# Kernel tuning notes

Measured on AMD Instinct MI355X. Metric: run time of the kernel, lower is better.

The kernel has to match this reference:

```python
import jax, jax.numpy as jnp
import numpy as np
from jax import lax

X_SIZE, Z_SIZE, H, GC, PD = 256, 64, 64, 16, 2
B, K, T = 256, 16, 50
LOG_SIG_MIN, LOG_SIG_MAX, LOG_P_MAX = -10.0, 10.0, 50.0
ZX = X_SIZE + Z_SIZE
LSTM_IN = ZX + PD


def setup_inputs() -> dict:
    key = jax.random.key(0)
    ks = jax.random.split(key, 24)
    s = lambda fan_in: 1.0 / np.sqrt(fan_in)
    u = lambda k, shape, sc: jax.random.uniform(k, shape, jnp.float32, -sc, sc)
    inp = {
        'x': jax.random.normal(ks[0], (B, X_SIZE), jnp.float32),
        'z_stacked': jax.random.normal(ks[1], (K, B, Z_SIZE), jnp.float32),
        'input_seqs': jax.random.normal(ks[2], (B, 8, 2, 2, 6), jnp.float32),
        'pred_seqs': jax.random.normal(ks[3], (B, T, 2, 2, 6), jnp.float32),
        # initial_h / initial_c linears: ZX -> H
        'Wh0': u(ks[4], (H, ZX), s(ZX)), 'bh0': u(ks[5], (H,), s(ZX)),
        'Wc0': u(ks[6], (H, ZX), s(ZX)), 'bc0': u(ks[7], (H,), s(ZX)),
        # LSTMCell: gates order i,f,g,o
        'Wih': u(ks[8], (4 * H, LSTM_IN), s(H)), 'Whh': u(ks[9], (4 * H, H), s(H)),
        'bih': u(ks[10], (4 * H,), s(H)), 'bhh': u(ks[11], (4 * H,), s(H)),
        # GMM parameter heads: H -> GC / GC*PD
        'Wpi': u(ks[12], (GC, H), s(H)), 'bpi': u(ks[13], (GC,), s(H)),
        'Wmu': u(ks[14], (GC * PD, H), s(H)), 'bmu': u(ks[15], (GC * PD,), s(H)),
        'Wls': u(ks[16], (GC * PD, H), s(H)), 'bls': u(ks[17], (GC * PD,), s(H)),
        'Wcorr': u(ks[18], (GC, H), s(H)), 'bcorr': u(ks[19], (GC,), s(H)),
        'n_z_samples': K,
    }
    return inp


def _gmm2d_log_prob(log_pis, mus, log_sigmas, corrs, value):
    # log_pis/corrs: [K,B,T,GC]; mus/log_sigmas: [K,B,T,GC*PD]; value: [B,T,PD]
    ls = jnp.clip(log_sigmas, LOG_SIG_MIN, LOG_SIG_MAX).reshape(K, B, T, GC, PD)
    mu = mus.reshape(K, B, T, GC, PD)
    dx = value[None, :, :, None, :] - mu                      # [K,B,T,GC,PD]
    zscore = dx * jnp.exp(-ls)                                # dx / sigma
    one_m_rho2 = 1.0 - corrs ** 2
    quad = (zscore[..., 0] ** 2 + zscore[..., 1] ** 2
            - 2.0 * corrs * zscore[..., 0] * zscore[..., 1])
    comp = (-jnp.log(2.0 * jnp.pi) - ls.sum(-1)
            - 0.5 * jnp.log(one_m_rho2) - 0.5 * quad / one_m_rho2)
    log_pi_n = jax.nn.log_softmax(log_pis, axis=-1)
    log_p_t = jax.nn.logsumexp(log_pi_n + comp, axis=-1)      # [K,B,T]
    return jnp.minimum(log_p_t, LOG_P_MAX)


def reference(x, z_stacked, input_seqs, pred_seqs,
              Wh0, bh0, Wc0, bc0, Wih, Whh, bih, bhh,
              Wpi, bpi, Wmu, bmu, Wls, bls, Wcorr, bcorr, n_z_samples):
    tgt_future = pred_seqs[:, :, 1, 1, 2:4]                   # [B,T,2]
    tgt_present = input_seqs[:, -1, 1, 1, 2:4]                # [B,2]
    z = z_stacked.reshape(-1, z_stacked.shape[-1])            # [K*B, z]
    zx = jnp.concatenate([z, jnp.tile(x, (n_z_samples, 1))], axis=1)  # [N, ZX]
    N = zx.shape[0]
    h0 = zx @ Wh0.T + bh0
    c0 = zx @ Wc0.T + bc0
    decode_inputs = jnp.concatenate([tgt_present[:, None, :], tgt_future[:, :T - 1, :]], axis=1)  # [B,T,2]
    inputs = jnp.concatenate([
        jnp.broadcast_to(zx[:, None, :], (N, T, ZX)),
        jnp.tile(decode_inputs, (n_z_samples, 1, 1))], axis=2)  # [N,T,ZX+2]

    def step(carry, xt):
        h, c = carry
        gates = xt @ Wih.T + bih + h @ Whh.T + bhh
        i, f, g, o = jnp.split(gates, 4, axis=-1)
        c = jax.nn.sigmoid(f) * c + jax.nn.sigmoid(i) * jnp.tanh(g)
        h = jax.nn.sigmoid(o) * jnp.tanh(c)
        return (h, c), h

    _, hs = lax.scan(step, (h0, c0), jnp.swapaxes(inputs, 0, 1))  # [T,N,H]
    hs = jnp.swapaxes(hs, 0, 1)                                   # [N,T,H]

    log_pis = (hs @ Wpi.T + bpi).reshape(K, B, T, GC)
    mus = (hs @ Wmu.T + bmu).reshape(K, B, T, GC * PD)
    log_sigmas = (hs @ Wls.T + bls).reshape(K, B, T, GC * PD)
    corrs = jnp.tanh(hs @ Wcorr.T + bcorr).reshape(K, B, T, GC)

    log_p_yt_xz = _gmm2d_log_prob(log_pis, mus, log_sigmas, corrs, tgt_future)
    return log_p_yt_xz.sum(axis=2)                                # [K,B]
```

## Files before the change

kernel.cpp:

```cpp
#include <hip/hip_runtime.h>


#define T_ 50
#define SPB 16
#define ZXS 324
#define HFS 72
#define PLS 100

typedef __attribute__((ext_vector_type(8))) short short8;
typedef __attribute__((ext_vector_type(4))) float f32x4;

#define MFMA(a, b, c) __builtin_amdgcn_mfma_f32_16x16x32_bf16(a, b, c, 0, 0, 0)

__device__ __forceinline__ float sigf(float x)  { return 1.0f / (1.0f + __expf(-x)); }
__device__ __forceinline__ float tanh_(float x) { return 1.0f - 2.0f / (__expf(2.0f * x) + 1.0f); }

__device__ __forceinline__ void splitf(float f, unsigned short& hi, unsigned short& lo) {
    unsigned b = __float_as_uint(f);
    hi = (unsigned short)(b >> 16);
    float fh = __uint_as_float(b & 0xffff0000u);
    lo = (unsigned short)(__float_as_uint(f - fh) >> 16);
}

__device__ __forceinline__ void pack8(const float* p, short8& hi, short8& lo) {
    #pragma unroll
    for (int e = 0; e < 8; ++e) {
        unsigned short h, l;
        splitf(p[e], h, l);
        hi[e] = (short)h; lo[e] = (short)l;
    }
}

__launch_bounds__(512, 1)
__global__ void decoder_kernel(
    const float* __restrict__ x,       const float* __restrict__ z,
    const float* __restrict__ inp_seqs,const float* __restrict__ pred_seqs,
    const float* __restrict__ Wh0,     const float* __restrict__ bh0,
    const float* __restrict__ Wc0,     const float* __restrict__ bc0,
    const float* __restrict__ Wih,     const float* __restrict__ Whh,
    const float* __restrict__ bih,     const float* __restrict__ bhh,
    const float* __restrict__ Wpi,     const float* __restrict__ bpi,
    const float* __restrict__ Wmu,     const float* __restrict__ bmu,
    const float* __restrict__ Wls,     const float* __restrict__ bls,
    const float* __restrict__ Wcorr,   const float* __restrict__ bcorr,
    float* __restrict__ out)
{
    __shared__ __align__(16) float smem[9248];
    float* ZXL = smem;
    float* PL0 = smem;
    float* PL1 = smem + 1600;
    unsigned short* HF0h = (unsigned short*)(smem + 5184);
    unsigned short* HF0l = HF0h + 1152;
    unsigned short* HF1h = HF0h + 2304;
    unsigned short* HF1l = HF0h + 3456;
    float* FUT = smem + 7616;
    float* PRS = smem + 9216;

    const int j = threadIdx.x;
    const int w = j >> 6;
    const int l = j & 63;
    const int g = l >> 4;
    const int c = l & 15;
    const int U = 16*(w & 3) + c;
    const int blk = blockIdx.x;

    for (int e = j; e < SPB*320; e += 512) {
        int s = e / 320, k = e - s*320;
        int n = blk*SPB + s, kk = n >> 8, b = n & 255;
        ZXL[s*ZXS + k] = (k < 64) ? z[(kk*256 + b)*64 + k] : x[b*256 + (k - 64)];
    }
    for (int e = j; e < T_*SPB; e += 512) {
        int t = e >> 4, s = e & 15;
        int b = (blk*SPB + s) & 255;
        float2 v = *reinterpret_cast<const float2*>(pred_seqs + b*1200 + t*24 + 20);
        FUT[t*32 + s*2] = v.x; FUT[t*32 + s*2 + 1] = v.y;
    }
    if (j < SPB) {
        int b = (blk*SPB + j) & 255;
        float2 v = *reinterpret_cast<const float2*>(inp_seqs + b*192 + 188);
        PRS[j*2] = v.x; PRS[j*2 + 1] = v.y;
    }
    __syncthreads();

    float cst[4];
    f32x4 gci, gcf, gcg, gco;
    float wdi0=0,wdi1=0,wdf0=0,wdf1=0,wdg0=0,wdg1=0,wdo0=0,wdo1=0;
    short8 WIh0,WIl0,WIh1,WIl1, WFh0,WFl0,WFh1,WFl1,
           WGh0,WGl0,WGh1,WGl1, WOh0,WOl0,WOh1,WOl1;
    short8 qAh0,qAl0,qAh1,qAl1, qBh0,qBl0,qBh1,qBl1;
    float biasA = 0.0f, biasB = 0.0f;
    int ptA = 0, nproj = 0;

    auto projrow = [&](int r3, const float*& p, float& b) {
        if      (r3 < 16) { p = Wpi   + r3*64;      b = bpi[r3]; }
        else if (r3 < 48) { p = Wmu   + (r3-16)*64; b = bmu[r3-16]; }
        else if (r3 < 80) { p = Wls   + (r3-48)*64; b = bls[r3-48]; }
        else              { p = Wcorr + (r3-80)*64; b = bcorr[r3-80]; }
    };

    if (w < 4) {
        const int R0 = U, R1 = 64 + U, R2 = 128 + U, R3 = 192 + U;
        {
            float bi_ = bih[R0] + bhh[R0], bf_ = bih[R1] + bhh[R1];
            float bg_ = bih[R2] + bhh[R2], bo_ = bih[R3] + bhh[R3];
            gci = (f32x4){bi_,bi_,bi_,bi_}; gcf = (f32x4){bf_,bf_,bf_,bf_};
            gcg = (f32x4){bg_,bg_,bg_,bg_}; gco = (f32x4){bo_,bo_,bo_,bo_};
        }
        float bc_ = bc0[U];
        f32x4 c0a = (f32x4){bc_, bc_, bc_, bc_};
        for (int ks = 0; ks < 10; ++ks) {
            int k0 = ks*32 + g*8;
            short8 ah, al, b0h,b0l, b1h,b1l, b2h,b2l, b3h,b3l, bch,bcl;
            pack8(&ZXL[c*ZXS + k0], ah, al);
            pack8(Wih + R0*322 + k0, b0h, b0l);
            pack8(Wih + R1*322 + k0, b1h, b1l);
            pack8(Wih + R2*322 + k0, b2h, b2l);
            pack8(Wih + R3*322 + k0, b3h, b3l);
            pack8(Wc0 + U*320 + k0, bch, bcl);
            gci = MFMA(ah,b0h,gci); gci = MFMA(ah,b0l,gci); gci = MFMA(al,b0h,gci);
            gcf = MFMA(ah,b1h,gcf); gcf = MFMA(ah,b1l,gcf); gcf = MFMA(al,b1h,gcf);
            gcg = MFMA(ah,b2h,gcg); gcg = MFMA(ah,b2l,gcg); gcg = MFMA(al,b2h,gcg);
            gco = MFMA(ah,b3h,gco); gco = MFMA(ah,b3l,gco); gco = MFMA(al,b3h,gco);
            c0a = MFMA(ah,bch,c0a); c0a = MFMA(ah,bcl,c0a); c0a = MFMA(al,bch,c0a);
        }
        #pragma unroll
        for (int r = 0; r < 4; ++r) cst[r] = c0a[r];
        wdi0 = Wih[R0*322+320]; wdi1 = Wih[R0*322+321];
        wdf0 = Wih[R1*322+320]; wdf1 = Wih[R1*322+321];
        wdg0 = Wih[R2*322+320]; wdg1 = Wih[R2*322+321];
        wdo0 = Wih[R3*322+320]; wdo1 = Wih[R3*322+321];
        pack8(Whh + R0*64 +      g*8, WIh0, WIl0); pack8(Whh + R0*64 + 32 + g*8, WIh1, WIl1);
        pack8(Whh + R1*64 +      g*8, WFh0, WFl0); pack8(Whh + R1*64 + 32 + g*8, WFh1, WFl1);
        pack8(Whh + R2*64 +      g*8, WGh0, WGl0); pack8(Whh + R2*64 + 32 + g*8, WGh1, WGl1);
        pack8(Whh + R3*64 +      g*8, WOh0, WOl0); pack8(Whh + R3*64 + 32 + g*8, WOh1, WOl1);
    } else {
        float bh_ = bh0[U];
        f32x4 h0a = (f32x4){bh_, bh_, bh_, bh_};
        for (int ks = 0; ks < 10; ++ks) {
            int k0 = ks*32 + g*8;
            short8 ah, al, bhh_, bhl_;
            pack8(&ZXL[c*ZXS + k0], ah, al);
            pack8(Wh0 + U*320 + k0, bhh_, bhl_);
            h0a = MFMA(ah,bhh_,h0a); h0a = MFMA(ah,bhl_,h0a); h0a = MFMA(al,bhh_,h0a);
        }
        #pragma unroll
        for (int r = 0; r < 4; ++r) {
            unsigned short hh, ll; splitf(h0a[r], hh, ll);
            HF0h[(4*g + r)*HFS + U] = hh;
            HF0l[(4*g + r)*HFS + U] = ll;
        }
        const int v = w - 4;
        nproj = (v < 2) ? 2 : 1;
        ptA = (v < 2) ? 2*v : (4 + (v - 2));
        {
            const float* p; projrow(ptA*16 + c, p, biasA);
            pack8(p +      g*8, qAh0, qAl0);
            pack8(p + 32 + g*8, qAh1, qAl1);
        }
        if (nproj == 2) {
            const float* p; projrow((ptA+1)*16 + c, p, biasB);
            pack8(p +      g*8, qBh0, qBl0);
            pack8(p + 32 + g*8, qBh1, qBl1);
        }
    }

    const int jj = j & 255;
    const int s3 = jj >> 4, g3 = jj & 15;
    float sum = 0.0f;

    auto do_proj = [&](const unsigned short* Hh, const unsigned short* Hl, float* PLw) {
        short8 ah0 = *reinterpret_cast<const short8*>(Hh + c*HFS +      g*8);
        short8 al0 = *reinterpret_cast<const short8*>(Hl + c*HFS +      g*8);
        short8 ah1 = *reinterpret_cast<const short8*>(Hh + c*HFS + 32 + g*8);
        short8 al1 = *reinterpret_cast<const short8*>(Hl + c*HFS + 32 + g*8);
        f32x4 pA = (f32x4){biasA, biasA, biasA, biasA};
        pA = MFMA(ah0,qAh0,pA); pA = MFMA(ah0,qAl0,pA); pA = MFMA(al0,qAh0,pA);
        pA = MFMA(ah1,qAh1,pA); pA = MFMA(ah1,qAl1,pA); pA = MFMA(al1,qAh1,pA);
        #pragma unroll
        for (int r = 0; r < 4; ++r) PLw[(4*g + r)*PLS + ptA*16 + c] = pA[r];
        if (nproj == 2) {
            f32x4 pB = (f32x4){biasB, biasB, biasB, biasB};
            pB = MFMA(ah0,qBh0,pB); pB = MFMA(ah0,qBl0,pB); pB = MFMA(al0,qBh0,pB);
            pB = MFMA(ah1,qBh1,pB); pB = MFMA(ah1,qBl1,pB); pB = MFMA(al1,qBh1,pB);
            #pragma unroll
            for (int r = 0; r < 4; ++r) PLw[(4*g + r)*PLS + (ptA+1)*16 + c] = pB[r];
        }
    };
    auto do_gmm = [&](const float* pl, const float* fut2) {
        const float* pls = pl + s3*PLS;
        float a_pi = pls[g3];
        float a_m0 = pls[16 + 2*g3], a_m1 = pls[17 + 2*g3];
        float l0   = pls[48 + 2*g3], l1   = pls[49 + 2*g3];
        float a_co = pls[80 + g3];
        float v0 = fut2[s3*2], v1 = fut2[s3*2 + 1];
        l0 = fminf(fmaxf(l0, -10.0f), 10.0f);
        l1 = fminf(fmaxf(l1, -10.0f), 10.0f);
        float z0 = (v0 - a_m0) * __expf(-l0);
        float z1 = (v1 - a_m1) * __expf(-l1);
        float ct = tanh_(a_co);
        float omr = 1.0f - ct*ct;
        float quad = z0*z0 + z1*z1 - 2.0f*ct*z0*z1;
        float comp = -1.8378770664093453f - (l0 + l1) - 0.5f*__logf(omr) - 0.5f*quad/omr;
        float a = a_pi + comp;
        float m1v = a, m2v = a_pi;
        #pragma unroll
        for (int off = 1; off < 16; off <<= 1) {
            m1v = fmaxf(m1v, __shfl_xor(m1v, off));
            m2v = fmaxf(m2v, __shfl_xor(m2v, off));
        }
        float e1 = __expf(a - m1v), e2 = __expf(a_pi - m2v);
        #pragma unroll
        for (int off = 1; off < 16; off <<= 1) {
            e1 += __shfl_xor(e1, off);
            e2 += __shfl_xor(e2, off);
        }
        float logp = (m1v + __logf(e1)) - (m2v + __logf(e2));
        sum += fminf(logp, 50.0f);
    };

    __syncthreads();

    for (int t = 0; t < T_; ++t) {
        const unsigned short* Hh = (t & 1) ? HF1h : HF0h;
        const unsigned short* Hl = (t & 1) ? HF1l : HF0l;
        if (w < 4) {
            unsigned short* Nh = (t & 1) ? HF0h : HF1h;
            unsigned short* Nl = (t & 1) ? HF0l : HF1l;
            short8 ah0 = *reinterpret_cast<const short8*>(Hh + c*HFS +      g*8);
            short8 al0 = *reinterpret_cast<const short8*>(Hl + c*HFS +      g*8);
            short8 ah1 = *reinterpret_cast<const short8*>(Hh + c*HFS + 32 + g*8);
            short8 al1 = *reinterpret_cast<const short8*>(Hl + c*HFS + 32 + g*8);
            const float* dptr = (t == 0) ? PRS : (FUT + (t-1)*32);
            f32x4 ai, af, ag, ao;
            #pragma unroll
            for (int r = 0; r < 4; ++r) {
                float2 dv = *reinterpret_cast<const float2*>(dptr + (4*g + r)*2);
                ai[r] = gci[r] + dv.x*wdi0 + dv.y*wdi1;
                af[r] = gcf[r] + dv.x*wdf0 + dv.y*wdf1;
                ag[r] = gcg[r] + dv.x*wdg0 + dv.y*wdg1;
                ao[r] = gco[r] + dv.x*wdo0 + dv.y*wdo1;
            }
            ai = MFMA(ah0,WIh0,ai); ai = MFMA(ah0,WIl0,ai); ai = MFMA(al0,WIh0,ai);
            ai = MFMA(ah1,WIh1,ai); ai = MFMA(ah1,WIl1,ai); ai = MFMA(al1,WIh1,ai);
            af = MFMA(ah0,WFh0,af); af = MFMA(ah0,WFl0,af); af = MFMA(al0,WFh0,af);
            af = MFMA(ah1,WFh1,af); af = MFMA(ah1,WFl1,af); af = MFMA(al1,WFh1,af);
            ag = MFMA(ah0,WGh0,ag); ag = MFMA(ah0,WGl0,ag); ag = MFMA(al0,WGh0,ag);
            ag = MFMA(ah1,WGh1,ag); ag = MFMA(ah1,WGl1,ag); ag = MFMA(al1,WGh1,ag);
            ao = MFMA(ah0,WOh0,ao); ao = MFMA(ah0,WOl0,ao); ao = MFMA(al0,WOh0,ao);
            ao = MFMA(ah1,WOh1,ao); ao = MFMA(ah1,WOl1,ao); ao = MFMA(al1,WOh1,ao);
            #pragma unroll
            for (int r = 0; r < 4; ++r) {
                float cc = sigf(af[r])*cst[r] + sigf(ai[r])*tanh_(ag[r]);
                cst[r] = cc;
                float hv = sigf(ao[r])*tanh_(cc);
                unsigned short hh, ll; splitf(hv, hh, ll);
                Nh[(4*g + r)*HFS + U] = hh;
                Nl[(4*g + r)*HFS + U] = ll;
            }
        } else {
            if (t >= 1) do_proj(Hh, Hl, (t & 1) ? PL1 : PL0);
            if (t >= 2) do_gmm((t & 1) ? PL0 : PL1, FUT + (t-2)*32);
        }
        __syncthreads();
    }

    if (w >= 4) {
        do_proj(HF0h, HF0l, PL0);
        do_gmm(PL1, FUT + 48*32);
    }
    __syncthreads();
    if (w >= 4) {
        do_gmm(PL0, FUT + 49*32);
        if (g3 == 0) out[blk*SPB + s3] = sum;
    }
}

extern "C" void kernel_launch(void* const* d_in, const int* in_sizes, int n_in,
                              void* d_out, int out_size, void* d_ws, size_t ws_size,
                              hipStream_t stream) {
    const float* x     = (const float*)d_in[0];
    const float* z     = (const float*)d_in[1];
    const float* iseq  = (const float*)d_in[2];
    const float* pseq  = (const float*)d_in[3];
    const float* Wh0   = (const float*)d_in[4];
    const float* bh0   = (const float*)d_in[5];
    const float* Wc0   = (const float*)d_in[6];
    const float* bc0   = (const float*)d_in[7];
    const float* Wih   = (const float*)d_in[8];
    const float* Whh   = (const float*)d_in[9];
    const float* bih   = (const float*)d_in[10];
    const float* bhh   = (const float*)d_in[11];
    const float* Wpi   = (const float*)d_in[12];
    const float* bpi   = (const float*)d_in[13];
    const float* Wmu   = (const float*)d_in[14];
    const float* bmu   = (const float*)d_in[15];
    const float* Wls   = (const float*)d_in[16];
    const float* bls   = (const float*)d_in[17];
    const float* Wcorr = (const float*)d_in[18];
    const float* bcorr = (const float*)d_in[19];
    float* out = (float*)d_out;

    decoder_kernel<<<256, 512, 0, stream>>>(x, z, iseq, pseq, Wh0, bh0, Wc0, bc0,
                                            Wih, Whh, bih, bhh, Wpi, bpi, Wmu, bmu,
                                            Wls, bls, Wcorr, bcorr, out);
}
```

Before: 95.87 us.

## Split decoder block into 12 waves: dedicated LSTM, projection, and GMM waves

Grows the block from 8 to 12 waves. The initial zx projections (input gates, h0, c0) are spread evenly across all 12 waves, with intermediate results staged through shared memory. In the time loop, 4 waves run the LSTM cell, 4 run the GMM parameter projections, and 4 run the GMM log-prob, where the old code had one set of waves doing both projection and GMM. This shortens the serial prologue and lets projection and GMM work overlap per step, at the cost of extra barriers, more shared-memory reuse, and changed launch bounds that may limit registers per thread.

New measurement: 98.50 us. +2.7%, slower.

```diff
diff --git a/kernel.cpp b/kernel.cpp
--- a/kernel.cpp
+++ b/kernel.cpp
@@ -2,15 +2,9 @@
 
 
 #define T_ 50
-#define SPB 16
-#define ZXS 324
-#define HFS 72
-#define PLS 100
-
 typedef __attribute__((ext_vector_type(8))) short short8;
 typedef __attribute__((ext_vector_type(4))) float f32x4;
-
-#define MFMA(a, b, c) __builtin_amdgcn_mfma_f32_16x16x32_bf16(a, b, c, 0, 0, 0)
+#define MFMA(a,b,c) __builtin_amdgcn_mfma_f32_16x16x32_bf16(a,b,c,0,0,0)
 
 __device__ __forceinline__ float sigf(float x)  { return 1.0f / (1.0f + __expf(-x)); }
 __device__ __forceinline__ float tanh_(float x) { return 1.0f - 2.0f / (__expf(2.0f * x) + 1.0f); }
@@ -31,7 +25,7 @@
     }
 }
 
-__launch_bounds__(512, 1)
+__launch_bounds__(768, 3)
 __global__ void decoder_kernel(
     const float* __restrict__ x,       const float* __restrict__ z,
     const float* __restrict__ inp_seqs,const float* __restrict__ pred_seqs,
@@ -45,149 +39,168 @@
     const float* __restrict__ Wcorr,   const float* __restrict__ bcorr,
     float* __restrict__ out)
 {
-    __shared__ __align__(16) float smem[9248];
+    __shared__ __align__(16) float smem[7488];
     float* ZXL = smem;
+    float* gcX = smem;
+    float* c0X = smem + 4096;
     float* PL0 = smem;
     float* PL1 = smem + 1600;
+    float* FUT = smem + 3200;
+    float* PRS = smem + 4800;
     unsigned short* HF0h = (unsigned short*)(smem + 5184);
     unsigned short* HF0l = HF0h + 1152;
     unsigned short* HF1h = HF0h + 2304;
     unsigned short* HF1l = HF0h + 3456;
-    float* FUT = smem + 7616;
-    float* PRS = smem + 9216;
 
     const int j = threadIdx.x;
     const int w = j >> 6;
     const int l = j & 63;
     const int g = l >> 4;
     const int c = l & 15;
-    const int U = 16*(w & 3) + c;
     const int blk = blockIdx.x;
 
-    for (int e = j; e < SPB*320; e += 512) {
+    for (int e = j; e < 16*320; e += 768) {
         int s = e / 320, k = e - s*320;
-        int n = blk*SPB + s, kk = n >> 8, b = n & 255;
-        ZXL[s*ZXS + k] = (k < 64) ? z[(kk*256 + b)*64 + k] : x[b*256 + (k - 64)];
-    }
-    for (int e = j; e < T_*SPB; e += 512) {
-        int t = e >> 4, s = e & 15;
-        int b = (blk*SPB + s) & 255;
-        float2 v = *reinterpret_cast<const float2*>(pred_seqs + b*1200 + t*24 + 20);
-        FUT[t*32 + s*2] = v.x; FUT[t*32 + s*2 + 1] = v.y;
-    }
-    if (j < SPB) {
-        int b = (blk*SPB + j) & 255;
-        float2 v = *reinterpret_cast<const float2*>(inp_seqs + b*192 + 188);
-        PRS[j*2] = v.x; PRS[j*2 + 1] = v.y;
-    }
-    __syncthreads();
-
+        int n = blk*16 + s, b = n & 255;
+        ZXL[s*324 + k] = (k < 64) ? z[n*64 + k] : x[b*256 + (k - 64)];
+    }
+    __syncthreads();
+
+    const int tA = w;
+    f32x4 accA, accB;
+    const float* srcA;
+    const float* srcB;
+    int tB = -1;
+    {
+        int qA_ = tA >> 2, ubA_ = tA & 3;
+        int gaA = qA_*64 + 16*ubA_ + c;
+        float bA = bih[gaA] + bhh[gaA];
+        accA = (f32x4){bA, bA, bA, bA};
+        srcA = Wih + gaA*322;
+        float bB;
+        if (w < 4) {
+            tB = 12 + w;
+            int qB_ = tB >> 2, ubB_ = tB & 3;
+            int gaB = qB_*64 + 16*ubB_ + c;
+            bB = bih[gaB] + bhh[gaB];
+            srcB = Wih + gaB*322;
+        } else if (w < 8) {
+            int u = 16*(w-4) + c;
+            bB = bh0[u];
+            srcB = Wh0 + u*320;
+        } else {
+            int u = 16*(w-8) + c;
+            bB = bc0[u];
+            srcB = Wc0 + u*320;
+        }
+        accB = (f32x4){bB, bB, bB, bB};
+    }
+    for (int ks = 0; ks < 10; ++ks) {
+        short8 ah, al;
+        pack8(&ZXL[c*324 + ks*32 + g*8], ah, al);
+        short8 b1h, b1l; pack8(srcA + ks*32 + g*8, b1h, b1l);
+        accA = MFMA(ah, b1h, accA); accA = MFMA(ah, b1l, accA); accA = MFMA(al, b1h, accA);
+        short8 b2h, b2l; pack8(srcB + ks*32 + g*8, b2h, b2l);
+        accB = MFMA(ah, b2h, accB); accB = MFMA(ah, b2l, accB); accB = MFMA(al, b2h, accB);
+    }
+    __syncthreads();
+
+    #pragma unroll
+    for (int r = 0; r < 4; ++r) gcX[tA*256 + (4*g + r)*16 + c] = accA[r];
+    if (w < 4) {
+        #pragma unroll
+        for (int r = 0; r < 4; ++r) gcX[tB*256 + (4*g + r)*16 + c] = accB[r];
+    } else if (w < 8) {
+        #pragma unroll
+        for (int r = 0; r < 4; ++r) {
+            unsigned short hh, ll; splitf(accB[r], hh, ll);
+            HF0h[(4*g + r)*72 + 16*(w-4) + c] = hh;
+            HF0l[(4*g + r)*72 + 16*(w-4) + c] = ll;
+        }
+    } else {
+        #pragma unroll
+        for (int r = 0; r < 4; ++r) c0X[(4*g + r)*64 + 16*(w-8) + c] = accB[r];
+    }
+    __syncthreads();
+
+    f32x4 gc[4];
     float cst[4];
-    f32x4 gci, gcf, gcg, gco;
-    float wdi0=0,wdi1=0,wdf0=0,wdf1=0,wdg0=0,wdg1=0,wdo0=0,wdo1=0;
-    short8 WIh0,WIl0,WIh1,WIl1, WFh0,WFl0,WFh1,WFl1,
-           WGh0,WGl0,WGh1,WGl1, WOh0,WOl0,WOh1,WOl1;
-    short8 qAh0,qAl0,qAh1,qAl1, qBh0,qBl0,qBh1,qBl1;
-    float biasA = 0.0f, biasB = 0.0f;
+    short8 WH[4][2], WL[4][2];
+    float wd0[4], wd1[4];
+    short8 qAh0, qAl0, qAh1, qAl1, qBh0, qBl0, qBh1, qBl1;
+    float pbA = 0.0f, pbB = 0.0f;
     int ptA = 0, nproj = 0;
-
-    auto projrow = [&](int r3, const float*& p, float& b) {
-        if      (r3 < 16) { p = Wpi   + r3*64;      b = bpi[r3]; }
-        else if (r3 < 48) { p = Wmu   + (r3-16)*64; b = bmu[r3-16]; }
-        else if (r3 < 80) { p = Wls   + (r3-48)*64; b = bls[r3-48]; }
-        else              { p = Wcorr + (r3-80)*64; b = bcorr[r3-80]; }
-    };
+    const int s3 = 4*(w - 8) + g;
+    const int g3 = c;
+    float sum = 0.0f;
 
     if (w < 4) {
-        const int R0 = U, R1 = 64 + U, R2 = 128 + U, R3 = 192 + U;
-        {
-            float bi_ = bih[R0] + bhh[R0], bf_ = bih[R1] + bhh[R1];
-            float bg_ = bih[R2] + bhh[R2], bo_ = bih[R3] + bhh[R3];
-            gci = (f32x4){bi_,bi_,bi_,bi_}; gcf = (f32x4){bf_,bf_,bf_,bf_};
-            gcg = (f32x4){bg_,bg_,bg_,bg_}; gco = (f32x4){bo_,bo_,bo_,bo_};
-        }
-        float bc_ = bc0[U];
-        f32x4 c0a = (f32x4){bc_, bc_, bc_, bc_};
-        for (int ks = 0; ks < 10; ++ks) {
-            int k0 = ks*32 + g*8;
-            short8 ah, al, b0h,b0l, b1h,b1l, b2h,b2l, b3h,b3l, bch,bcl;
-            pack8(&ZXL[c*ZXS + k0], ah, al);
-            pack8(Wih + R0*322 + k0, b0h, b0l);
-            pack8(Wih + R1*322 + k0, b1h, b1l);
-            pack8(Wih + R2*322 + k0, b2h, b2l);
-            pack8(Wih + R3*322 + k0, b3h, b3l);
-            pack8(Wc0 + U*320 + k0, bch, bcl);
-            gci = MFMA(ah,b0h,gci); gci = MFMA(ah,b0l,gci); gci = MFMA(al,b0h,gci);
-            gcf = MFMA(ah,b1h,gcf); gcf = MFMA(ah,b1l,gcf); gcf = MFMA(al,b1h,gcf);
-            gcg = MFMA(ah,b2h,gcg); gcg = MFMA(ah,b2l,gcg); gcg = MFMA(al,b2h,gcg);
-            gco = MFMA(ah,b3h,gco); gco = MFMA(ah,b3l,gco); gco = MFMA(al,b3h,gco);
-            c0a = MFMA(ah,bch,c0a); c0a = MFMA(ah,bcl,c0a); c0a = MFMA(al,bch,c0a);
-        }
-        #pragma unroll
-        for (int r = 0; r < 4; ++r) cst[r] = c0a[r];
-        wdi0 = Wih[R0*322+320]; wdi1 = Wih[R0*322+321];
-        wdf0 = Wih[R1*322+320]; wdf1 = Wih[R1*322+321];
-        wdg0 = Wih[R2*322+320]; wdg1 = Wih[R2*322+321];
-        wdo0 = Wih[R3*322+320]; wdo1 = Wih[R3*322+321];
-        pack8(Whh + R0*64 +      g*8, WIh0, WIl0); pack8(Whh + R0*64 + 32 + g*8, WIh1, WIl1);
-        pack8(Whh + R1*64 +      g*8, WFh0, WFl0); pack8(Whh + R1*64 + 32 + g*8, WFh1, WFl1);
-        pack8(Whh + R2*64 +      g*8, WGh0, WGl0); pack8(Whh + R2*64 + 32 + g*8, WGh1, WGl1);
-        pack8(Whh + R3*64 +      g*8, WOh0, WOl0); pack8(Whh + R3*64 + 32 + g*8, WOh1, WOl1);
-    } else {
-        float bh_ = bh0[U];
-        f32x4 h0a = (f32x4){bh_, bh_, bh_, bh_};
-        for (int ks = 0; ks < 10; ++ks) {
-            int k0 = ks*32 + g*8;
-            short8 ah, al, bhh_, bhl_;
-            pack8(&ZXL[c*ZXS + k0], ah, al);
-            pack8(Wh0 + U*320 + k0, bhh_, bhl_);
-            h0a = MFMA(ah,bhh_,h0a); h0a = MFMA(ah,bhl_,h0a); h0a = MFMA(al,bhh_,h0a);
-        }
-        #pragma unroll
-        for (int r = 0; r < 4; ++r) {
-            unsigned short hh, ll; splitf(h0a[r], hh, ll);
-            HF0h[(4*g + r)*HFS + U] = hh;
-            HF0l[(4*g + r)*HFS + U] = ll;
-        }
-        const int v = w - 4;
+        #pragma unroll
+        for (int q = 0; q < 4; ++q) {
+            #pragma unroll
+            for (int r = 0; r < 4; ++r)
+                gc[q][r] = gcX[(q*4 + w)*256 + (4*g + r)*16 + c];
+            int ga = q*64 + 16*w + c;
+            pack8(Whh + ga*64 +      g*8, WH[q][0], WL[q][0]);
+            pack8(Whh + ga*64 + 32 + g*8, WH[q][1], WL[q][1]);
+            wd0[q] = Wih[ga*322 + 320];
+            wd1[q] = Wih[ga*322 + 321];
+        }
+        #pragma unroll
+        for (int r = 0; r < 4; ++r) cst[r] = c0X[(4*g + r)*64 + 16*w + c];
+    } else if (w < 8) {
+        int v = w - 4;
         nproj = (v < 2) ? 2 : 1;
-        ptA = (v < 2) ? 2*v : (4 + (v - 2));
-        {
-            const float* p; projrow(ptA*16 + c, p, biasA);
-            pack8(p +      g*8, qAh0, qAl0);
-            pack8(p + 32 + g*8, qAh1, qAl1);
-        }
+        ptA = (v < 2) ? 2*v : 4 + (v - 2);
+        auto projrow = [&](int r3, const float*& p, float& b) {
+            if      (r3 < 16) { p = Wpi   + r3*64;      b = bpi[r3]; }
+            else if (r3 < 48) { p = Wmu   + (r3-16)*64; b = bmu[r3-16]; }
+            else if (r3 < 80) { p = Wls   + (r3-48)*64; b = bls[r3-48]; }
+            else              { p = Wcorr + (r3-80)*64; b = bcorr[r3-80]; }
+        };
+        const float* p;
+        projrow(ptA*16 + c, p, pbA);
+        pack8(p +      g*8, qAh0, qAl0);
+        pack8(p + 32 + g*8, qAh1, qAl1);
         if (nproj == 2) {
-            const float* p; projrow((ptA+1)*16 + c, p, biasB);
+            projrow((ptA+1)*16 + c, p, pbB);
             pack8(p +      g*8, qBh0, qBl0);
             pack8(p + 32 + g*8, qBh1, qBl1);
         }
     }
-
-    const int jj = j & 255;
-    const int s3 = jj >> 4, g3 = jj & 15;
-    float sum = 0.0f;
+    __syncthreads();
+
+    for (int e = j; e < T_*32; e += 768) {
+        int t = e >> 5, rem = e & 31, s = rem >> 1;
+        int b = (blk*16 + s) & 255;
+        FUT[e] = pred_seqs[b*1200 + t*24 + 20 + (rem & 1)];
+    }
+    if (j < 32) {
+        int b = (blk*16 + (j >> 1)) & 255;
+        PRS[j] = inp_seqs[b*192 + 188 + (j & 1)];
+    }
+    __syncthreads();
 
     auto do_proj = [&](const unsigned short* Hh, const unsigned short* Hl, float* PLw) {
-        short8 ah0 = *reinterpret_cast<const short8*>(Hh + c*HFS +      g*8);
-        short8 al0 = *reinterpret_cast<const short8*>(Hl + c*HFS +      g*8);
-        short8 ah1 = *reinterpret_cast<const short8*>(Hh + c*HFS + 32 + g*8);
-        short8 al1 = *reinterpret_cast<const short8*>(Hl + c*HFS + 32 + g*8);
-        f32x4 pA = (f32x4){biasA, biasA, biasA, biasA};
-        pA = MFMA(ah0,qAh0,pA); pA = MFMA(ah0,qAl0,pA); pA = MFMA(al0,qAh0,pA);
-        pA = MFMA(ah1,qAh1,pA); pA = MFMA(ah1,qAl1,pA); pA = MFMA(al1,qAh1,pA);
-        #pragma unroll
-        for (int r = 0; r < 4; ++r) PLw[(4*g + r)*PLS + ptA*16 + c] = pA[r];
+        short8 ah0 = *reinterpret_cast<const short8*>(Hh + c*72 +      g*8);
+        short8 al0 = *reinterpret_cast<const short8*>(Hl + c*72 +      g*8);
+        short8 ah1 = *reinterpret_cast<const short8*>(Hh + c*72 + 32 + g*8);
+        short8 al1 = *reinterpret_cast<const short8*>(Hl + c*72 + 32 + g*8);
+        f32x4 pA = (f32x4){pbA, pbA, pbA, pbA};
+        pA = MFMA(ah0, qAh0, pA); pA = MFMA(ah0, qAl0, pA); pA = MFMA(al0, qAh0, pA);
+        pA = MFMA(ah1, qAh1, pA); pA = MFMA(ah1, qAl1, pA); pA = MFMA(al1, qAh1, pA);
+        #pragma unroll
+        for (int r = 0; r < 4; ++r) PLw[(4*g + r)*100 + ptA*16 + c] = pA[r];
         if (nproj == 2) {
-            f32x4 pB = (f32x4){biasB, biasB, biasB, biasB};
-            pB = MFMA(ah0,qBh0,pB); pB = MFMA(ah0,qBl0,pB); pB = MFMA(al0,qBh0,pB);
-            pB = MFMA(ah1,qBh1,pB); pB = MFMA(ah1,qBl1,pB); pB = MFMA(al1,qBh1,pB);
-            #pragma unroll
-            for (int r = 0; r < 4; ++r) PLw[(4*g + r)*PLS + (ptA+1)*16 + c] = pB[r];
+            f32x4 pB = (f32x4){pbB, pbB, pbB, pbB};
+            pB = MFMA(ah0, qBh0, pB); pB = MFMA(ah0, qBl0, pB); pB = MFMA(al0, qBh0, pB);
+            pB = MFMA(ah1, qBh1, pB); pB = MFMA(ah1, qBl1, pB); pB = MFMA(al1, qBh1, pB);
+            #pragma unroll
+            for (int r = 0; r < 4; ++r) PLw[(4*g + r)*100 + (ptA+1)*16 + c] = pB[r];
         }
     };
     auto do_gmm = [&](const float* pl, const float* fut2) {
-        const float* pls = pl + s3*PLS;
+        const float* pls = pl + s3*100;
         float a_pi = pls[g3];
         float a_m0 = pls[16 + 2*g3], a_m1 = pls[17 + 2*g3];
         float l0   = pls[48 + 2*g3], l1   = pls[49 + 2*g3];
@@ -218,60 +231,57 @@
         sum += fminf(logp, 50.0f);
     };
 
-    __syncthreads();
-
     for (int t = 0; t < T_; ++t) {
         const unsigned short* Hh = (t & 1) ? HF1h : HF0h;
         const unsigned short* Hl = (t & 1) ? HF1l : HF0l;
         if (w < 4) {
             unsigned short* Nh = (t & 1) ? HF0h : HF1h;
             unsigned short* Nl = (t & 1) ? HF0l : HF1l;
-            short8 ah0 = *reinterpret_cast<const short8*>(Hh + c*HFS +      g*8);
-            short8 al0 = *reinterpret_cast<const short8*>(Hl + c*HFS +      g*8);
-            short8 ah1 = *reinterpret_cast<const short8*>(Hh + c*HFS + 32 + g*8);
-            short8 al1 = *reinterpret_cast<const short8*>(Hl + c*HFS + 32 + g*8);
+            short8 ah0 = *reinterpret_cast<const short8*>(Hh + c*72 +      g*8);
+            short8 al0 = *reinterpret_cast<const short8*>(Hl + c*72 +      g*8);
+            short8 ah1 = *reinterpret_cast<const short8*>(Hh + c*72 + 32 + g*8);
+            short8 al1 = *reinterpret_cast<const short8*>(Hl + c*72 + 32 + g*8);
             const float* dptr = (t == 0) ? PRS : (FUT + (t-1)*32);
-            f32x4 ai, af, ag, ao;
+            float2 dv[4];
+            #pragma unroll
+            for (int r = 0; r < 4; ++r)
+                dv[r] = *reinterpret_cast<const float2*>(dptr + (4*g + r)*2);
+            f32x4 aq[4];
+            #pragma unroll
+            for (int q = 0; q < 4; ++q) {
+                #pragma unroll
+                for (int r = 0; r < 4; ++r)
+                    aq[q][r] = gc[q][r] + dv[r].x*wd0[q] + dv[r].y*wd1[q];
+                aq[q] = MFMA(ah0, WH[q][0], aq[q]);
+                aq[q] = MFMA(ah0, WL[q][0], aq[q]);
+                aq[q] = MFMA(al0, WH[q][0], aq[q]);
+                aq[q] = MFMA(ah1, WH[q][1], aq[q]);
+                aq[q] = MFMA(ah1, WL[q][1], aq[q]);
+                aq[q] = MFMA(al1, WH[q][1], aq[q]);
+            }
             #pragma unroll
             for (int r = 0; r < 4; ++r) {
-                float2 dv = *reinterpret_cast<const float2*>(dptr + (4*g + r)*2);
-                ai[r] = gci[r] + dv.x*wdi0 + dv.y*wdi1;
-                af[r] = gcf[r] + dv.x*wdf0 + dv.y*wdf1;
-                ag[r] = gcg[r] + dv.x*wdg0 + dv.y*wdg1;
-                ao[r] = gco[r] + dv.x*wdo0 + dv.y*wdo1;
+                float cc = sigf(aq[1][r])*cst[r] + sigf(aq[0][r])*tanh_(aq[2][r]);
+                cst[r] = cc;
+                float hv = sigf(aq[3][r])*tanh_(cc);
+                unsigned short hh, ll; splitf(hv, hh, ll);
+                Nh[(4*g + r)*72 + 16*w + c] = hh;
+                Nl[(4*g + r)*72 + 16*w + c] = ll;
             }
-            ai = MFMA(ah0,WIh0,ai); ai = MFMA(ah0,WIl0,ai); ai = MFMA(al0,WIh0,ai);
-            ai = MFMA(ah1,WIh1,ai); ai = MFMA(ah1,WIl1,ai); ai = MFMA(al1,WIh1,ai);
-            af = MFMA(ah0,WFh0,af); af = MFMA(ah0,WFl0,af); af = MFMA(al0,WFh0,af);
-            af = MFMA(ah1,WFh1,af); af = MFMA(ah1,WFl1,af); af = MFMA(al1,WFh1,af);
-            ag = MFMA(ah0,WGh0,ag); ag = MFMA(ah0,WGl0,ag); ag = MFMA(al0,WGh0,ag);
-            ag = MFMA(ah1,WGh1,ag); ag = MFMA(ah1,WGl1,ag); ag = MFMA(al1,WGh1,ag);
-            ao = MFMA(ah0,WOh0,ao); ao = MFMA(ah0,WOl0,ao); ao = MFMA(al0,WOh0,ao);
-            ao = MFMA(ah1,WOh1,ao); ao = MFMA(ah1,WOl1,ao); ao = MFMA(al1,WOh1,ao);
-            #pragma unroll
-            for (int r = 0; r < 4; ++r) {
-                float cc = sigf(af[r])*cst[r] + sigf(ai[r])*tanh_(ag[r]);
-                cst[r] = cc;
-                float hv = sigf(ao[r])*tanh_(cc);
-                unsigned short hh, ll; splitf(hv, hh, ll);
-                Nh[(4*g + r)*HFS + U] = hh;
-                Nl[(4*g + r)*HFS + U] = ll;
-            }
+        } else if (w < 8) {
+            if (t >= 1) do_proj(Hh, Hl, (t & 1) ? PL1 : PL0);
         } else {
-            if (t >= 1) do_proj(Hh, Hl, (t & 1) ? PL1 : PL0);
             if (t >= 2) do_gmm((t & 1) ? PL0 : PL1, FUT + (t-2)*32);
         }
         __syncthreads();
     }
 
-    if (w >= 4) {
-        do_proj(HF0h, HF0l, PL0);
-        do_gmm(PL1, FUT + 48*32);
-    }
-    __syncthreads();
-    if (w >= 4) {
+    if (w >= 4 && w < 8) do_proj(HF0h, HF0l, PL0);
+    if (w >= 8) do_gmm(PL1, FUT + 48*32);
+    __syncthreads();
+    if (w >= 8) {
         do_gmm(PL0, FUT + 49*32);
-        if (g3 == 0) out[blk*SPB + s3] = sum;
+        if (g3 == 0) out[blk*16 + s3] = sum;
     }
 }
 
@@ -300,7 +310,7 @@
     const float* bcorr = (const float*)d_in[19];
     float* out = (float*)d_out;
 
-    decoder_kernel<<<256, 512, 0, stream>>>(x, z, iseq, pseq, Wh0, bh0, Wc0, bc0,
+    decoder_kernel<<<256, 768, 0, stream>>>(x, z, iseq, pseq, Wh0, bh0, Wc0, bc0,
                                             Wih, Whh, bih, bhh, Wpi, bpi, Wmu, bmu,
                                             Wls, bls, Wcorr, bcorr, out);
 }
```
